# Optimization experiments

Hardware: AMD Instinct MI355X
Metric: run time of the kernel (lower is better)

The kernel has to match this reference:

```python
import jax, jax.numpy as jnp
import numpy as np

B, LC, I, H, O, T = 512, 512, 64, 100, 64, 256


def setup_inputs() -> dict:
    key = jax.random.key(0)
    ks = jax.random.split(key, 10)
    context = jax.random.normal(ks[0], (B, LC, I), dtype=jnp.float32)
    context_lengths = jnp.clip(jax.random.randint(ks[1], (B,), 0, LC), 1, LC)
    s_e = 1.0 / np.sqrt(I)   # embed init scale (pytorch Linear default)
    s_h = 1.0 / np.sqrt(H)
    u = lambda k, shp, s: jax.random.uniform(k, shp, jnp.float32, -s, s)
    return {
        "context": context,
        "context_lengths": context_lengths,
        "t_steps": T,
        "W_embed": u(ks[2], (H, I), s_e), "b_embed": u(ks[3], (H,), s_e),
        "W_ih": u(ks[4], (3 * H, H), s_h), "b_ih": u(ks[5], (3 * H,), s_h),
        "W_hh": u(ks[6], (3 * H, H), s_h), "b_hh": u(ks[7], (3 * H,), s_h),
        "W_proj": u(ks[8], (O, H), s_h), "b_proj": u(ks[9], (O,), s_h),
    }


def _gru_cell(h, x_pre, W_hh, b_hh):
    # x_pre: precomputed x @ W_ih.T + b_ih, shape [B, 3H]
    gh = h @ W_hh.T + b_hh
    ri, zi, ni = jnp.split(x_pre, 3, axis=-1)
    rh, zh, nh = jnp.split(gh, 3, axis=-1)
    r = jax.nn.sigmoid(ri + rh)
    z = jax.nn.sigmoid(zi + zh)
    n = jnp.tanh(ni + r * nh)
    return (1.0 - z) * n + z * h


def reference(context, context_lengths, t_steps, W_embed, b_embed,
              W_ih, W_hh, b_ih, b_hh, W_proj, b_proj):
    Bc = context.shape[0]
    # ---- encode ----
    x = context @ W_embed.T + b_embed                      # [B, Lc, H]
    x_pre = x @ W_ih.T + b_ih                              # [B, Lc, 3H] (input gates precomputed)

    def enc_step(h, xp):
        h = _gru_cell(h, xp, W_hh, b_hh)
        return h, h

    h_init = jnp.zeros((Bc, W_hh.shape[1]), context.dtype)
    _, hs = jax.lax.scan(enc_step, h_init, jnp.swapaxes(x_pre, 0, 1))  # hs: [Lc, B, H]
    h0 = hs[context_lengths - 1, jnp.arange(Bc)]           # last valid hidden per example

    z0 = h0 @ W_proj.T + b_proj                            # [B, O]

    def dec_step(carry, _):
        h, z = carry
        xp = (z @ W_embed.T + b_embed) @ W_ih.T + b_ih
        h = _gru_cell(h, xp, W_hh, b_hh)
        z = h @ W_proj.T + b_proj
        return (h, z), z

    _, zs = jax.lax.scan(dec_step, (h0, z0), None, length=t_steps)  # [T, B, O]
    out = jnp.concatenate([z0[None], zs], axis=0)          # [T+1, B, O]
    return jnp.swapaxes(out, 0, 1)                         # [B, T+1, O]
```

## Files before the change

kernel.cpp:

```cpp
#include <hip/hip_runtime.h>


#define B_  512
#define LC_ 512
#define I_  64
#define H_  100
#define O_  64
#define T_  256
#define H3  300

#define WS_WC   0
#define WS_BC   19200
#define WS_WD   19500
#define WS_BD   49500
#define WS_PERM 49800

typedef float v2f __attribute__((ext_vector_type(2)));

__global__ __launch_bounds__(64) void prep1(const float* __restrict__ Wih,
                                            const float* __restrict__ bih,
                                            const float* __restrict__ Wemb,
                                            const float* __restrict__ bemb,
                                            float* __restrict__ ws) {
    int j = blockIdx.x;
    int i = threadIdx.x;
    float acc = 0.f;
    for (int k = 0; k < H_; ++k) acc += Wih[j * H_ + k] * Wemb[k * I_ + i];
    ws[WS_WC + j * I_ + i] = acc;
    if (i == 0) {
        float b = bih[j];
        for (int k = 0; k < H_; ++k) b += Wih[j * H_ + k] * bemb[k];
        ws[WS_BC + j] = b;
    }
}

__global__ __launch_bounds__(128) void prep2(const float* __restrict__ Wproj,
                                             const float* __restrict__ bproj,
                                             float* __restrict__ ws) {
    int j = blockIdx.x;
    int u = threadIdx.x;
    const float* Wc = ws + WS_WC;
    if (u < H_) {
        float acc = 0.f;
        for (int o = 0; o < O_; ++o) acc += Wc[j * I_ + o] * Wproj[o * H_ + u];
        ws[WS_WD + j * H_ + u] = acc;
    }
    if (u == 0) {
        float b = ws[WS_BC + j];
        for (int o = 0; o < O_; ++o) b += Wc[j * I_ + o] * bproj[o];
        ws[WS_BD + j] = b;
    }
}

__global__ __launch_bounds__(512) void sortk(const int* __restrict__ lens,
                                             int* __restrict__ perm) {
    __shared__ int sl[B_];
    int tid = threadIdx.x;
    sl[tid] = lens[tid];
    __syncthreads();
    int li = sl[tid];
    int rank = 0;
    for (int j = 0; j < B_; ++j) {
        int lj = sl[j];
        rank += (lj > li) || (lj == li && j < tid);
    }
    perm[rank] = tid;
}

__device__ __forceinline__ float sigm_(float x) { return 1.f / (1.f + __expf(-x)); }
__device__ __forceinline__ float tanh_(float x) {
    float t = __expf(-2.f * fabsf(x));
    float r = (1.f - t) / (1.f + t);
    return (x >= 0.f) ? r : -r;
}

template <int CTRL>
__device__ __forceinline__ float dppmov_(float x) {
    return __int_as_float(
        __builtin_amdgcn_mov_dpp(__float_as_int(x), CTRL, 0xF, 0xF, true));
}
__device__ __forceinline__ float red4_(float a) {
    a += dppmov_<0xB1>(a);
    a += dppmov_<0x4E>(a);
    return a;
}

__device__ __forceinline__ float dotH_(const v2f* __restrict__ w2, float w1,
                                       const v2f* __restrict__ hv2, float h24) {
    v2f a = {0.f, 0.f};
    #pragma unroll
    for (int j = 0; j < 12; ++j) a = w2[j] * hv2[j] + a;
    return red4_(fmaf(w1, h24, a.x + a.y));
}
__device__ __forceinline__ float dotC_(const v2f* __restrict__ w2,
                                       const v2f* __restrict__ cv2) {
    v2f a = {0.f, 0.f};
    #pragma unroll
    for (int j = 0; j < 8; ++j) a = w2[j] * cv2[j] + a;
    return red4_(a.x + a.y);
}

__global__ __attribute__((amdgpu_flat_work_group_size(512, 512)))
__attribute__((amdgpu_waves_per_eu(2, 2)))
void rnn8(const float* __restrict__ ctx, const int* __restrict__ lens,
          const float* __restrict__ Whh, const float* __restrict__ bhh,
          const float* __restrict__ Wproj, const float* __restrict__ bproj,
          const float* __restrict__ ws, float* __restrict__ out) {

    const int tid = threadIdx.x;
    const int l   = tid & 3;
    const int g   = tid >> 2;
    const bool wl = (l == 0);

    const int* perm = (const int*)(ws + WS_PERM);
    const int e0 = perm[blockIdx.x];
    const int e1 = perm[511 - blockIdx.x];
    const int len0 = lens[e0], len1 = lens[e1];

    __shared__ __align__(16) float sh[2][112];
    __shared__ __align__(16) float sctx[2][64];
    __shared__ float sdot[2][672];
    __shared__ float sbh[H3], sbx[H3];

    const bool p2hh = (g < 44);
    const bool p4a  = (g < 88);
    const bool p5a  = (g < 24);

    v2f   w2[6][12];
    float w1[6];
    {
        const float* r0 = Whh + g * H_ + 25 * l;
        const float* r1 = Whh + (128 + g) * H_ + 25 * l;
        #pragma unroll
        for (int j = 0; j < 12; ++j) {
            w2[0][j] = v2f{r0[2 * j], r0[2 * j + 1]};
            w2[1][j] = v2f{r1[2 * j], r1[2 * j + 1]};
        }
        w1[0] = r0[24]; w1[1] = r1[24];
        if (p2hh) {
            const float* r2 = Whh + (256 + g) * H_ + 25 * l;
            #pragma unroll
            for (int j = 0; j < 12; ++j) w2[2][j] = v2f{r2[2 * j], r2[2 * j + 1]};
            w1[2] = r2[24];
        } else {
            const float* r2 = ws + WS_WC + (g - 44) * I_ + 16 * l;
            #pragma unroll
            for (int j = 0; j < 8; ++j) w2[2][j] = v2f{r2[2 * j], r2[2 * j + 1]};
        }
        const float* r3 = ws + WS_WC + (84 + g) * I_ + 16 * l;
        #pragma unroll
        for (int j = 0; j < 8; ++j) w2[3][j] = v2f{r3[2 * j], r3[2 * j + 1]};
        if (p4a) {
            const float* r4 = ws + WS_WC + (212 + g) * I_ + 16 * l;
            #pragma unroll
            for (int j = 0; j < 8; ++j) w2[4][j] = v2f{r4[2 * j], r4[2 * j + 1]};
        }
    }

    const int ge = (tid >= 100);
    const int gi = tid - (ge ? 100 : 0);
    const int hs = 28 * (gi / 25) + (gi % 25);
    const int lenG = ge ? len1 : len0;
    float hreg = 0.f;

    const int oe = (tid >> 6) & 1;
    const int oo = tid & 63;
    float* oute = out + (size_t)(oe ? e1 : e0) * (T_ + 1) * O_;
    float bpr = 0.f;
    if (tid >= 256 && tid < 384) bpr = bproj[oo];

    const int pe = (tid >> 4) & 1;
    const int pi = tid & 15;
    const float4* pctx = (const float4*)(ctx + (size_t)(pe ? e1 : e0) * LC_ * I_);
    const int lenP = pe ? len1 : len0;

    if (tid < 224) ((float*)sh)[tid] = 0.f;
    if (tid < H3) { sbh[tid] = bhh[tid]; sbx[tid] = (ws + WS_BC)[tid]; }
    if (tid >= 384 && tid < 416) *(float4*)&sctx[pe][4 * pi] = pctx[pi];
    __syncthreads();

    for (int t = 0; t < len0; ++t) {
        float4 pf;
        const bool hp = (tid >= 384 && tid < 416) && (t + 1 < lenP);
        if (hp) pf = pctx[(t + 1) * 16 + pi];

        #pragma unroll
        for (int e = 0; e < 2; ++e) {
            if (e == 0 || t < len1) {
                v2f hv2[12], cv2[8];
                float h24;
                #pragma unroll
                for (int q = 0; q < 6; ++q) {
                    float4 f = *(const float4*)&sh[e][28 * l + 4 * q];
                    hv2[2 * q]     = v2f{f.x, f.y};
                    hv2[2 * q + 1] = v2f{f.z, f.w};
                }
                h24 = sh[e][28 * l + 24];
                #pragma unroll
                for (int q = 0; q < 4; ++q) {
                    float4 f = *(const float4*)&sctx[e][16 * l + 4 * q];
                    cv2[2 * q]     = v2f{f.x, f.y};
                    cv2[2 * q + 1] = v2f{f.z, f.w};
                }

                float a0 = dotH_(w2[0], w1[0], hv2, h24);
                float a1 = dotH_(w2[1], w1[1], hv2, h24);
                float a2 = p2hh ? dotH_(w2[2], w1[2], hv2, h24) : dotC_(w2[2], cv2);
                float a3 = dotC_(w2[3], cv2);
                if (wl) {
                    sdot[e][g] = a0;
                    sdot[e][128 + g] = a1;
                    sdot[e][256 + g] = a2;
                    sdot[e][384 + g] = a3;
                }
                if (p4a) {
                    float a4 = dotC_(w2[4], cv2);
                    if (wl) sdot[e][512 + g] = a4;
                }
            }
        }
        __syncthreads();
        if (tid < 200 && t < lenG) {
            const float* sd = sdot[ge];
            float gr = sd[gi]       + sbh[gi];
            float gz = sd[gi + 100] + sbh[gi + 100];
            float gn = sd[gi + 200] + sbh[gi + 200];
            float xr = sd[gi + 300] + sbx[gi];
            float xz = sd[gi + 400] + sbx[gi + 100];
            float xn = sd[gi + 500] + sbx[gi + 200];
            float r = sigm_(xr + gr);
            float z = sigm_(xz + gz);
            float n = tanh_(xn + r * gn);
            hreg = (1.f - z) * n + z * hreg;
            sh[ge][hs] = hreg;
        }
        if (hp) *(float4*)&sctx[pe][4 * pi] = pf;
        __syncthreads();
    }

    {
        if (!p2hh) {
            const float* r2 = ws + WS_WD + (g - 44) * H_ + 25 * l;
            #pragma unroll
            for (int j = 0; j < 12; ++j) w2[2][j] = v2f{r2[2 * j], r2[2 * j + 1]};
            w1[2] = r2[24];
        }
        const float* r3 = ws + WS_WD + (84 + g) * H_ + 25 * l;
        #pragma unroll
        for (int j = 0; j < 12; ++j) w2[3][j] = v2f{r3[2 * j], r3[2 * j + 1]};
        w1[3] = r3[24];
        const float* r4 = p4a ? (ws + WS_WD + (212 + g) * H_ + 25 * l)
                              : (Wproj + (g - 88) * H_ + 25 * l);
        #pragma unroll
        for (int j = 0; j < 12; ++j) w2[4][j] = v2f{r4[2 * j], r4[2 * j + 1]};
        w1[4] = r4[24];
        if (p5a) {
            const float* r5 = Wproj + (40 + g) * H_ + 25 * l;
            #pragma unroll
            for (int j = 0; j < 12; ++j) w2[5][j] = v2f{r5[2 * j], r5[2 * j + 1]};
            w1[5] = r5[24];
        }
    }
    if (tid < H3) sbx[tid] = (ws + WS_BD)[tid];

    for (int t = 0; t <= T_; ++t) {
        #pragma unroll
        for (int e = 0; e < 2; ++e) {
            v2f hv2[12];
            float h24;
            #pragma unroll
            for (int q = 0; q < 6; ++q) {
                float4 f = *(const float4*)&sh[e][28 * l + 4 * q];
                hv2[2 * q]     = v2f{f.x, f.y};
                hv2[2 * q + 1] = v2f{f.z, f.w};
            }
            h24 = sh[e][28 * l + 24];

            float a0 = dotH_(w2[0], w1[0], hv2, h24);
            float a1 = dotH_(w2[1], w1[1], hv2, h24);
            float a2 = dotH_(w2[2], w1[2], hv2, h24);
            float a3 = dotH_(w2[3], w1[3], hv2, h24);
            float a4 = dotH_(w2[4], w1[4], hv2, h24);
            if (wl) {
                sdot[e][g] = a0;
                sdot[e][128 + g] = a1;
                sdot[e][256 + g] = a2;
                sdot[e][384 + g] = a3;
                sdot[e][512 + g] = a4;
            }
            if (p5a) {
                float a5 = dotH_(w2[5], w1[5], hv2, h24);
                if (wl) sdot[e][640 + g] = a5;
            }
        }
        __syncthreads();
        if (tid >= 256 && tid < 384) {
            oute[t * O_ + oo] = sdot[oe][600 + oo] + bpr;
        }
        if (t == T_) break;
        if (tid < 200) {
            const float* sd = sdot[ge];
            float gr = sd[gi]       + sbh[gi];
            float gz = sd[gi + 100] + sbh[gi + 100];
            float gn = sd[gi + 200] + sbh[gi + 200];
            float xr = sd[gi + 300] + sbx[gi];
            float xz = sd[gi + 400] + sbx[gi + 100];
            float xn = sd[gi + 500] + sbx[gi + 200];
            float r = sigm_(xr + gr);
            float z = sigm_(xz + gz);
            float n = tanh_(xn + r * gn);
            hreg = (1.f - z) * n + z * hreg;
            sh[ge][hs] = hreg;
        }
        __syncthreads();
    }
}

extern "C" void kernel_launch(void* const* d_in, const int* in_sizes, int n_in,
                              void* d_out, int out_size, void* d_ws, size_t ws_size,
                              hipStream_t stream) {
    (void)in_sizes; (void)n_in; (void)out_size; (void)ws_size;
    const float* ctx  = (const float*)d_in[0];
    const int*   lens = (const int*)d_in[1];
    const float* Wemb = (const float*)d_in[3];
    const float* bemb = (const float*)d_in[4];
    const float* Wih  = (const float*)d_in[5];
    const float* bih  = (const float*)d_in[6];
    const float* Whh  = (const float*)d_in[7];
    const float* bhh  = (const float*)d_in[8];
    const float* Wpr  = (const float*)d_in[9];
    const float* bpr  = (const float*)d_in[10];
    float* ws  = (float*)d_ws;
    float* out = (float*)d_out;

    prep1<<<H3, 64, 0, stream>>>(Wih, bih, Wemb, bemb, ws);
    prep2<<<H3, 128, 0, stream>>>(Wpr, bpr, ws);
    sortk<<<1, 512, 0, stream>>>(lens, (int*)(ws + WS_PERM));
    rnn8<<<256, 512, 0, stream>>>(ctx, lens, Whh, bhh, Wpr, bpr, ws, out);
}
```

Before: 729.2 us.

## Interleave two sequences' dot and gate phases to overlap gate math with dots

Restructures both the encoder and decoder loops so that the gate update for one sequence runs in the same barrier interval as the matrix-vector dots for the other sequence, in a staggered ping-pong. The context prefetch buffer is double-buffered per sequence to fit the new schedule. The intent is to hide the serial gate/activation phase, which previously sat between barriers with most threads idle, behind the dot-product work. It adds bookkeeping for the offset between the two sequences and a tail step, and the barrier count per step stays the same.

After: 742.4 us. Within noise of the previous version (+1.8%).

```diff
diff --git a/kernel.cpp b/kernel.cpp
--- a/kernel.cpp
+++ b/kernel.cpp
@@ -102,7 +102,7 @@
 
 __global__ __attribute__((amdgpu_flat_work_group_size(512, 512)))
 __attribute__((amdgpu_waves_per_eu(2, 2)))
-void rnn8(const float* __restrict__ ctx, const int* __restrict__ lens,
+void rnn9(const float* __restrict__ ctx, const int* __restrict__ lens,
           const float* __restrict__ Whh, const float* __restrict__ bhh,
           const float* __restrict__ Wproj, const float* __restrict__ bproj,
           const float* __restrict__ ws, float* __restrict__ out) {
@@ -118,7 +118,7 @@
     const int len0 = lens[e0], len1 = lens[e1];
 
     __shared__ __align__(16) float sh[2][112];
-    __shared__ __align__(16) float sctx[2][64];
+    __shared__ __align__(16) float sctx[2][2][64];
     __shared__ float sdot[2][672];
     __shared__ float sbh[H3], sbx[H3];
 
@@ -160,81 +160,121 @@
     const int ge = (tid >= 100);
     const int gi = tid - (ge ? 100 : 0);
     const int hs = 28 * (gi / 25) + (gi % 25);
-    const int lenG = ge ? len1 : len0;
     float hreg = 0.f;
 
-    const int oe = (tid >> 6) & 1;
+    const bool iso = (tid >= 256 && tid < 320);
     const int oo = tid & 63;
-    float* oute = out + (size_t)(oe ? e1 : e0) * (T_ + 1) * O_;
+    float* oute0 = out + (size_t)e0 * (T_ + 1) * O_;
+    float* oute1 = out + (size_t)e1 * (T_ + 1) * O_;
     float bpr = 0.f;
-    if (tid >= 256 && tid < 384) bpr = bproj[oo];
-
-    const int pe = (tid >> 4) & 1;
+    if (iso) bpr = bproj[oo];
+
+    const bool isp = (tid >= 384 && tid < 400);
     const int pi = tid & 15;
-    const float4* pctx = (const float4*)(ctx + (size_t)(pe ? e1 : e0) * LC_ * I_);
-    const int lenP = pe ? len1 : len0;
+    const float4* pctx0 = (const float4*)(ctx + (size_t)e0 * LC_ * I_);
+    const float4* pctx1 = (const float4*)(ctx + (size_t)e1 * LC_ * I_);
 
     if (tid < 224) ((float*)sh)[tid] = 0.f;
     if (tid < H3) { sbh[tid] = bhh[tid]; sbx[tid] = (ws + WS_BC)[tid]; }
-    if (tid >= 384 && tid < 416) *(float4*)&sctx[pe][4 * pi] = pctx[pi];
+    if (isp) {
+        *(float4*)&sctx[0][0][4 * pi] = pctx0[pi];
+        *(float4*)&sctx[1][0][4 * pi] = pctx1[pi];
+    }
     __syncthreads();
 
+    auto gate_ = [&](int e) {
+        const float* sd = sdot[e];
+        float gr = sd[gi]       + sbh[gi];
+        float gz = sd[gi + 100] + sbh[gi + 100];
+        float gn = sd[gi + 200] + sbh[gi + 200];
+        float xr = sd[gi + 300] + sbx[gi];
+        float xz = sd[gi + 400] + sbx[gi + 100];
+        float xn = sd[gi + 500] + sbx[gi + 200];
+        float r = sigm_(xr + gr);
+        float z = sigm_(xz + gz);
+        float n = tanh_(xn + r * gn);
+        hreg = (1.f - z) * n + z * hreg;
+        sh[e][hs] = hreg;
+    };
+    auto dotsEnc = [&](int e, int buf) {
+        v2f hv2[12], cv2[8];
+        float h24;
+        #pragma unroll
+        for (int q = 0; q < 6; ++q) {
+            float4 f = *(const float4*)&sh[e][28 * l + 4 * q];
+            hv2[2 * q]     = v2f{f.x, f.y};
+            hv2[2 * q + 1] = v2f{f.z, f.w};
+        }
+        h24 = sh[e][28 * l + 24];
+        #pragma unroll
+        for (int q = 0; q < 4; ++q) {
+            float4 f = *(const float4*)&sctx[e][buf][16 * l + 4 * q];
+            cv2[2 * q]     = v2f{f.x, f.y};
+            cv2[2 * q + 1] = v2f{f.z, f.w};
+        }
+        float a0 = dotH_(w2[0], w1[0], hv2, h24);
+        float a1 = dotH_(w2[1], w1[1], hv2, h24);
+        float a2 = p2hh ? dotH_(w2[2], w1[2], hv2, h24) : dotC_(w2[2], cv2);
+        float a3 = dotC_(w2[3], cv2);
+        if (wl) {
+            sdot[e][g] = a0;
+            sdot[e][128 + g] = a1;
+            sdot[e][256 + g] = a2;
+            sdot[e][384 + g] = a3;
+        }
+        if (p4a) {
+            float a4 = dotC_(w2[4], cv2);
+            if (wl) sdot[e][512 + g] = a4;
+        }
+    };
+    auto dotsDec = [&](int e) {
+        v2f hv2[12];
+        float h24;
+        #pragma unroll
+        for (int q = 0; q < 6; ++q) {
+            float4 f = *(const float4*)&sh[e][28 * l + 4 * q];
+            hv2[2 * q]     = v2f{f.x, f.y};
+            hv2[2 * q + 1] = v2f{f.z, f.w};
+        }
+        h24 = sh[e][28 * l + 24];
+        float a0 = dotH_(w2[0], w1[0], hv2, h24);
+        float a1 = dotH_(w2[1], w1[1], hv2, h24);
+        float a2 = dotH_(w2[2], w1[2], hv2, h24);
+        float a3 = dotH_(w2[3], w1[3], hv2, h24);
+        float a4 = dotH_(w2[4], w1[4], hv2, h24);
+        if (wl) {
+            sdot[e][g] = a0;
+            sdot[e][128 + g] = a1;
+            sdot[e][256 + g] = a2;
+            sdot[e][384 + g] = a3;
+            sdot[e][512 + g] = a4;
+        }
+        if (p5a) {
+            float a5 = dotH_(w2[5], w1[5], hv2, h24);
+            if (wl) sdot[e][640 + g] = a5;
+        }
+    };
+
+    float4 pf;
+
     for (int t = 0; t < len0; ++t) {
-        float4 pf;
-        const bool hp = (tid >= 384 && tid < 416) && (t + 1 < lenP);
-        if (hp) pf = pctx[(t + 1) * 16 + pi];
-
-        #pragma unroll
-        for (int e = 0; e < 2; ++e) {
-            if (e == 0 || t < len1) {
-                v2f hv2[12], cv2[8];
-                float h24;
-                #pragma unroll
-                for (int q = 0; q < 6; ++q) {
-                    float4 f = *(const float4*)&sh[e][28 * l + 4 * q];
-                    hv2[2 * q]     = v2f{f.x, f.y};
-                    hv2[2 * q + 1] = v2f{f.z, f.w};
-                }
-                h24 = sh[e][28 * l + 24];
-                #pragma unroll
-                for (int q = 0; q < 4; ++q) {
-                    float4 f = *(const float4*)&sctx[e][16 * l + 4 * q];
-                    cv2[2 * q]     = v2f{f.x, f.y};
-                    cv2[2 * q + 1] = v2f{f.z, f.w};
-                }
-
-                float a0 = dotH_(w2[0], w1[0], hv2, h24);
-                float a1 = dotH_(w2[1], w1[1], hv2, h24);
-                float a2 = p2hh ? dotH_(w2[2], w1[2], hv2, h24) : dotC_(w2[2], cv2);
-                float a3 = dotC_(w2[3], cv2);
-                if (wl) {
-                    sdot[e][g] = a0;
-                    sdot[e][128 + g] = a1;
-                    sdot[e][256 + g] = a2;
-                    sdot[e][384 + g] = a3;
-                }
-                if (p4a) {
-                    float a4 = dotC_(w2[4], cv2);
-                    if (wl) sdot[e][512 + g] = a4;
-                }
-            }
-        }
-        __syncthreads();
-        if (tid < 200 && t < lenG) {
-            const float* sd = sdot[ge];
-            float gr = sd[gi]       + sbh[gi];
-            float gz = sd[gi + 100] + sbh[gi + 100];
-            float gn = sd[gi + 200] + sbh[gi + 200];
-            float xr = sd[gi + 300] + sbx[gi];
-            float xz = sd[gi + 400] + sbx[gi + 100];
-            float xn = sd[gi + 500] + sbx[gi + 200];
-            float r = sigm_(xr + gr);
-            float z = sigm_(xz + gz);
-            float n = tanh_(xn + r * gn);
-            hreg = (1.f - z) * n + z * hreg;
-            sh[ge][hs] = hreg;
-        }
-        if (hp) *(float4*)&sctx[pe][4 * pi] = pf;
+        if (isp) {
+            if (t >= 1 && t < len1) *(float4*)&sctx[1][t & 1][4 * pi] = pf;
+            if (t + 1 < len0) pf = pctx0[(t + 1) * 16 + pi];
+        }
+        if (ge && tid < 200 && t >= 1 && t - 1 < len1) gate_(1);
+        dotsEnc(0, t & 1);
+        __syncthreads();
+        if (isp) {
+            if (t + 1 < len0) *(float4*)&sctx[0][(t + 1) & 1][4 * pi] = pf;
+            if (t + 1 < len1) pf = pctx1[(t + 1) * 16 + pi];
+        }
+        if (tid < 100) gate_(0);
+        if (t < len1) dotsEnc(1, t & 1);
+        __syncthreads();
+    }
+    if (len1 == len0) {
+        if (ge && tid < 200) gate_(1);
         __syncthreads();
     }
 
@@ -264,56 +304,18 @@
     if (tid < H3) sbx[tid] = (ws + WS_BD)[tid];
 
     for (int t = 0; t <= T_; ++t) {
-        #pragma unroll
-        for (int e = 0; e < 2; ++e) {
-            v2f hv2[12];
-            float h24;
-            #pragma unroll
-            for (int q = 0; q < 6; ++q) {
-                float4 f = *(const float4*)&sh[e][28 * l + 4 * q];
-                hv2[2 * q]     = v2f{f.x, f.y};
-                hv2[2 * q + 1] = v2f{f.z, f.w};
-            }
-            h24 = sh[e][28 * l + 24];
-
-            float a0 = dotH_(w2[0], w1[0], hv2, h24);
-            float a1 = dotH_(w2[1], w1[1], hv2, h24);
-            float a2 = dotH_(w2[2], w1[2], hv2, h24);
-            float a3 = dotH_(w2[3], w1[3], hv2, h24);
-            float a4 = dotH_(w2[4], w1[4], hv2, h24);
-            if (wl) {
-                sdot[e][g] = a0;
-                sdot[e][128 + g] = a1;
-                sdot[e][256 + g] = a2;
-                sdot[e][384 + g] = a3;
-                sdot[e][512 + g] = a4;
-            }
-            if (p5a) {
-                float a5 = dotH_(w2[5], w1[5], hv2, h24);
-                if (wl) sdot[e][640 + g] = a5;
-            }
-        }
-        __syncthreads();
-        if (tid >= 256 && tid < 384) {
-            oute[t * O_ + oo] = sdot[oe][600 + oo] + bpr;
-        }
-        if (t == T_) break;
-        if (tid < 200) {
-            const float* sd = sdot[ge];
-            float gr = sd[gi]       + sbh[gi];
-            float gz = sd[gi + 100] + sbh[gi + 100];
-            float gn = sd[gi + 200] + sbh[gi + 200];
-            float xr = sd[gi + 300] + sbx[gi];
-            float xz = sd[gi + 400] + sbx[gi + 100];
-            float xn = sd[gi + 500] + sbx[gi + 200];
-            float r = sigm_(xr + gr);
-            float z = sigm_(xz + gz);
-            float n = tanh_(xn + r * gn);
-            hreg = (1.f - z) * n + z * hreg;
-            sh[ge][hs] = hreg;
-        }
-        __syncthreads();
-    }
+        if (t >= 1) {
+            if (ge && tid < 200) gate_(1);
+            if (iso) oute1[(t - 1) * O_ + oo] = sdot[1][600 + oo] + bpr;
+        }
+        dotsDec(0);
+        __syncthreads();
+        if (tid < 100 && t < T_) gate_(0);
+        if (iso) oute0[t * O_ + oo] = sdot[0][600 + oo] + bpr;
+        dotsDec(1);
+        __syncthreads();
+    }
+    if (iso) oute1[T_ * O_ + oo] = sdot[1][600 + oo] + bpr;
 }
 
 extern "C" void kernel_launch(void* const* d_in, const int* in_sizes, int n_in,
@@ -336,5 +338,5 @@
     prep1<<<H3, 64, 0, stream>>>(Wih, bih, Wemb, bemb, ws);
     prep2<<<H3, 128, 0, stream>>>(Wpr, bpr, ws);
     sortk<<<1, 512, 0, stream>>>(lens, (int*)(ws + WS_PERM));
-    rnn8<<<256, 512, 0, stream>>>(ctx, lens, Whh, bhh, Wpr, bpr, ws, out);
-}
+    rnn9<<<256, 512, 0, stream>>>(ctx, lens, Whh, bhh, Wpr, bpr, ws, out);
+}
```

## Fuse gate math into per-row dot threads with double-buffered hidden state

Applied to the files above, without the earlier changes.

Restructures the recurrent kernel so each 4-lane group owns one hidden unit and holds all six gate weight rows plus biases in registers. The group computes the gate nonlinearities and the new hidden value directly, with no shared-memory dot-product scratch. Hidden state and context are double-buffered, which cuts each timestep from two barriers to one. The projection output moves to a separate set of 64 threads that compute it alongside the next step. The cost is higher register pressure from the extra weight rows and redundant gate math across the four lanes.

Measured after the change: 1.382 ms. 89.5% more time.

```diff
diff --git a/kernel.cpp b/kernel.cpp
--- a/kernel.cpp
+++ b/kernel.cpp
@@ -102,10 +102,10 @@
 
 __global__ __attribute__((amdgpu_flat_work_group_size(512, 512)))
 __attribute__((amdgpu_waves_per_eu(2, 2)))
-void rnn8(const float* __restrict__ ctx, const int* __restrict__ lens,
-          const float* __restrict__ Whh, const float* __restrict__ bhh,
-          const float* __restrict__ Wproj, const float* __restrict__ bproj,
-          const float* __restrict__ ws, float* __restrict__ out) {
+void rnn10(const float* __restrict__ ctx, const int* __restrict__ lens,
+           const float* __restrict__ Whh, const float* __restrict__ bhh,
+           const float* __restrict__ Wproj, const float* __restrict__ bproj,
+           const float* __restrict__ ws, float* __restrict__ out) {
 
     const int tid = threadIdx.x;
     const int l   = tid & 3;
@@ -117,200 +117,199 @@
     const int e1 = perm[511 - blockIdx.x];
     const int len0 = lens[e0], len1 = lens[e1];
 
-    __shared__ __align__(16) float sh[2][112];
-    __shared__ __align__(16) float sctx[2][64];
-    __shared__ float sdot[2][672];
-    __shared__ float sbh[H3], sbx[H3];
-
-    const bool p2hh = (g < 44);
-    const bool p4a  = (g < 88);
-    const bool p5a  = (g < 24);
-
-    v2f   w2[6][12];
-    float w1[6];
-    {
-        const float* r0 = Whh + g * H_ + 25 * l;
-        const float* r1 = Whh + (128 + g) * H_ + 25 * l;
+    __shared__ __align__(16) float sh[2][2][112];
+    __shared__ __align__(16) float sctx[2][2][64];
+
+    const bool isG  = (g < 112);
+    const bool real = (g < 100);
+    const int  hslot = real ? (28 * (g / 25) + (g % 25)) : 0;
+
+    v2f   wh[3][12]; float wh1[3]; float bh[3];
+    v2f   wx[3][12]; float wx1[3]; float bx[3];
+    float hreg0 = 0.f, hreg1 = 0.f;
+    v2f   wp[4][12]; float wp1[4]; float bp[4];
+
+    if (isG) {
         #pragma unroll
-        for (int j = 0; j < 12; ++j) {
-            w2[0][j] = v2f{r0[2 * j], r0[2 * j + 1]};
-            w2[1][j] = v2f{r1[2 * j], r1[2 * j + 1]};
-        }
-        w1[0] = r0[24]; w1[1] = r1[24];
-        if (p2hh) {
-            const float* r2 = Whh + (256 + g) * H_ + 25 * l;
+        for (int r = 0; r < 3; ++r) {
+            if (real) {
+                const float* p = Whh + (g + 100 * r) * H_ + 25 * l;
+                #pragma unroll
+                for (int j = 0; j < 12; ++j) wh[r][j] = v2f{p[2 * j], p[2 * j + 1]};
+                wh1[r] = p[24];
+                bh[r]  = bhh[g + 100 * r];
+                const float* pc = ws + WS_WC + (g + 100 * r) * I_ + 16 * l;
+                #pragma unroll
+                for (int j = 0; j < 8; ++j) wx[r][j] = v2f{pc[2 * j], pc[2 * j + 1]};
+                bx[r] = ws[WS_BC + g + 100 * r];
+            } else {
+                #pragma unroll
+                for (int j = 0; j < 12; ++j) { wh[r][j] = v2f{0.f, 0.f}; wx[r][j] = v2f{0.f, 0.f}; }
+                wh1[r] = 0.f; wx1[r] = 0.f; bh[r] = 0.f; bx[r] = 0.f;
+            }
+        }
+    } else {
+        const int k = g - 112;
+        #pragma unroll
+        for (int r = 0; r < 4; ++r) {
+            const float* p = Wproj + (k + 16 * r) * H_ + 25 * l;
             #pragma unroll
-            for (int j = 0; j < 12; ++j) w2[2][j] = v2f{r2[2 * j], r2[2 * j + 1]};
-            w1[2] = r2[24];
-        } else {
-            const float* r2 = ws + WS_WC + (g - 44) * I_ + 16 * l;
-            #pragma unroll
-            for (int j = 0; j < 8; ++j) w2[2][j] = v2f{r2[2 * j], r2[2 * j + 1]};
-        }
-        const float* r3 = ws + WS_WC + (84 + g) * I_ + 16 * l;
+            for (int j = 0; j < 12; ++j) wp[r][j] = v2f{p[2 * j], p[2 * j + 1]};
+            wp1[r] = p[24];
+            bp[r]  = bproj[k + 16 * r];
+        }
+    }
+
+    const int pl = tid - 448;
+    const int pe = (pl >> 4) & 1;
+    const int pi = pl & 15;
+    const float4* pc0 = (const float4*)(ctx + (size_t)e0 * LC_ * I_);
+    const float4* pc1 = (const float4*)(ctx + (size_t)e1 * LC_ * I_);
+    const float4* pcm = pe ? pc1 : pc0;
+    const int lenp = pe ? len1 : len0;
+    float4 pf = {0.f, 0.f, 0.f, 0.f};
+
+    float* oute0 = out + (size_t)e0 * (T_ + 1) * O_;
+    float* oute1 = out + (size_t)e1 * (T_ + 1) * O_;
+
+    if (tid < 448) ((float*)sh)[tid] = 0.f;
+    if (!isG && pl < 32) {
+        *(float4*)&sctx[pe][0][4 * pi] = pcm[pi];
+        if (1 < lenp) pf = pcm[16 + pi];
+    }
+    __syncthreads();
+
+    auto loadH = [&](int e, int b, v2f* hv2, float& h24) {
         #pragma unroll
-        for (int j = 0; j < 8; ++j) w2[3][j] = v2f{r3[2 * j], r3[2 * j + 1]};
-        if (p4a) {
-            const float* r4 = ws + WS_WC + (212 + g) * I_ + 16 * l;
-            #pragma unroll
-            for (int j = 0; j < 8; ++j) w2[4][j] = v2f{r4[2 * j], r4[2 * j + 1]};
-        }
-    }
-
-    const int ge = (tid >= 100);
-    const int gi = tid - (ge ? 100 : 0);
-    const int hs = 28 * (gi / 25) + (gi % 25);
-    const int lenG = ge ? len1 : len0;
-    float hreg = 0.f;
-
-    const int oe = (tid >> 6) & 1;
-    const int oo = tid & 63;
-    float* oute = out + (size_t)(oe ? e1 : e0) * (T_ + 1) * O_;
-    float bpr = 0.f;
-    if (tid >= 256 && tid < 384) bpr = bproj[oo];
-
-    const int pe = (tid >> 4) & 1;
-    const int pi = tid & 15;
-    const float4* pctx = (const float4*)(ctx + (size_t)(pe ? e1 : e0) * LC_ * I_);
-    const int lenP = pe ? len1 : len0;
-
-    if (tid < 224) ((float*)sh)[tid] = 0.f;
-    if (tid < H3) { sbh[tid] = bhh[tid]; sbx[tid] = (ws + WS_BC)[tid]; }
-    if (tid >= 384 && tid < 416) *(float4*)&sctx[pe][4 * pi] = pctx[pi];
-    __syncthreads();
+        for (int q = 0; q < 6; ++q) {
+            float4 f = *(const float4*)&sh[e][b][28 * l + 4 * q];
+            hv2[2 * q]     = v2f{f.x, f.y};
+            hv2[2 * q + 1] = v2f{f.z, f.w};
+        }
+        h24 = sh[e][b][28 * l + 24];
+    };
 
     for (int t = 0; t < len0; ++t) {
-        float4 pf;
-        const bool hp = (tid >= 384 && tid < 416) && (t + 1 < lenP);
-        if (hp) pf = pctx[(t + 1) * 16 + pi];
-
-        #pragma unroll
-        for (int e = 0; e < 2; ++e) {
-            if (e == 0 || t < len1) {
-                v2f hv2[12], cv2[8];
-                float h24;
-                #pragma unroll
-                for (int q = 0; q < 6; ++q) {
-                    float4 f = *(const float4*)&sh[e][28 * l + 4 * q];
-                    hv2[2 * q]     = v2f{f.x, f.y};
-                    hv2[2 * q + 1] = v2f{f.z, f.w};
-                }
-                h24 = sh[e][28 * l + 24];
+        const int rb = t & 1, wb = rb ^ 1;
+        if (isG) {
+            {
+                v2f hv2[12], cv2[8]; float h24;
+                loadH(0, rb, hv2, h24);
                 #pragma unroll
                 for (int q = 0; q < 4; ++q) {
-                    float4 f = *(const float4*)&sctx[e][16 * l + 4 * q];
+                    float4 f = *(const float4*)&sctx[0][rb][16 * l + 4 * q];
                     cv2[2 * q]     = v2f{f.x, f.y};
                     cv2[2 * q + 1] = v2f{f.z, f.w};
                 }
-
-                float a0 = dotH_(w2[0], w1[0], hv2, h24);
-                float a1 = dotH_(w2[1], w1[1], hv2, h24);
-                float a2 = p2hh ? dotH_(w2[2], w1[2], hv2, h24) : dotC_(w2[2], cv2);
-                float a3 = dotC_(w2[3], cv2);
-                if (wl) {
-                    sdot[e][g] = a0;
-                    sdot[e][128 + g] = a1;
-                    sdot[e][256 + g] = a2;
-                    sdot[e][384 + g] = a3;
+                float gr = dotH_(wh[0], wh1[0], hv2, h24) + bh[0];
+                float gz = dotH_(wh[1], wh1[1], hv2, h24) + bh[1];
+                float gn = dotH_(wh[2], wh1[2], hv2, h24) + bh[2];
+                float xr = dotC_(wx[0], cv2) + bx[0];
+                float xz = dotC_(wx[1], cv2) + bx[1];
+                float xn = dotC_(wx[2], cv2) + bx[2];
+                float r = sigm_(xr + gr);
+                float z = sigm_(xz + gz);
+                float n = tanh_(xn + r * gn);
+                hreg0 = (1.f - z) * n + z * hreg0;
+                if (wl && real) sh[0][wb][hslot] = hreg0;
+            }
+            if (t < len1) {
+                v2f hv2[12], cv2[8]; float h24;
+                loadH(1, rb, hv2, h24);
+                #pragma unroll
+                for (int q = 0; q < 4; ++q) {
+                    float4 f = *(const float4*)&sctx[1][rb][16 * l + 4 * q];
+                    cv2[2 * q]     = v2f{f.x, f.y};
+                    cv2[2 * q + 1] = v2f{f.z, f.w};
                 }
-                if (p4a) {
-                    float a4 = dotC_(w2[4], cv2);
-                    if (wl) sdot[e][512 + g] = a4;
+                float gr = dotH_(wh[0], wh1[0], hv2, h24) + bh[0];
+                float gz = dotH_(wh[1], wh1[1], hv2, h24) + bh[1];
+                float gn = dotH_(wh[2], wh1[2], hv2, h24) + bh[2];
+                float xr = dotC_(wx[0], cv2) + bx[0];
+                float xz = dotC_(wx[1], cv2) + bx[1];
+                float xn = dotC_(wx[2], cv2) + bx[2];
+                float r = sigm_(xr + gr);
+                float z = sigm_(xz + gz);
+                float n = tanh_(xn + r * gn);
+                hreg1 = (1.f - z) * n + z * hreg1;
+                if (wl && real) sh[1][wb][hslot] = hreg1;
+            }
+        } else if (pl < 32) {
+            if (t + 1 < lenp) *(float4*)&sctx[pe][wb][4 * pi] = pf;
+            if (t + 2 < lenp) pf = pcm[(t + 2) * 16 + pi];
+        }
+        __syncthreads();
+    }
+
+    if (isG && real) {
+        #pragma unroll
+        for (int r = 0; r < 3; ++r) {
+            const float* p = ws + WS_WD + (g + 100 * r) * H_ + 25 * l;
+            #pragma unroll
+            for (int j = 0; j < 12; ++j) wx[r][j] = v2f{p[2 * j], p[2 * j + 1]};
+            wx1[r] = p[24];
+            bx[r]  = ws[WS_BD + g + 100 * r];
+        }
+    }
+
+    const int p0 = len0 & 1, p1 = len1 & 1;
+    for (int t = 0; t <= T_; ++t) {
+        const int rb0 = (p0 + t) & 1, rb1 = (p1 + t) & 1;
+        if (isG) {
+            if (t < T_) {
+                {
+                    v2f hv2[12]; float h24;
+                    loadH(0, rb0, hv2, h24);
+                    float gr = dotH_(wh[0], wh1[0], hv2, h24) + bh[0];
+                    float gz = dotH_(wh[1], wh1[1], hv2, h24) + bh[1];
+                    float gn = dotH_(wh[2], wh1[2], hv2, h24) + bh[2];
+                    float xr = dotH_(wx[0], wx1[0], hv2, h24) + bx[0];
+                    float xz = dotH_(wx[1], wx1[1], hv2, h24) + bx[1];
+                    float xn = dotH_(wx[2], wx1[2], hv2, h24) + bx[2];
+                    float r = sigm_(xr + gr);
+                    float z = sigm_(xz + gz);
+                    float n = tanh_(xn + r * gn);
+                    hreg0 = (1.f - z) * n + z * hreg0;
+                    if (wl && real) sh[0][rb0 ^ 1][hslot] = hreg0;
                 }
-            }
-        }
-        __syncthreads();
-        if (tid < 200 && t < lenG) {
-            const float* sd = sdot[ge];
-            float gr = sd[gi]       + sbh[gi];
-            float gz = sd[gi + 100] + sbh[gi + 100];
-            float gn = sd[gi + 200] + sbh[gi + 200];
-            float xr = sd[gi + 300] + sbx[gi];
-            float xz = sd[gi + 400] + sbx[gi + 100];
-            float xn = sd[gi + 500] + sbx[gi + 200];
-            float r = sigm_(xr + gr);
-            float z = sigm_(xz + gz);
-            float n = tanh_(xn + r * gn);
-            hreg = (1.f - z) * n + z * hreg;
-            sh[ge][hs] = hreg;
-        }
-        if (hp) *(float4*)&sctx[pe][4 * pi] = pf;
-        __syncthreads();
-    }
-
-    {
-        if (!p2hh) {
-            const float* r2 = ws + WS_WD + (g - 44) * H_ + 25 * l;
-            #pragma unroll
-            for (int j = 0; j < 12; ++j) w2[2][j] = v2f{r2[2 * j], r2[2 * j + 1]};
-            w1[2] = r2[24];
-        }
-        const float* r3 = ws + WS_WD + (84 + g) * H_ + 25 * l;
-        #pragma unroll
-        for (int j = 0; j < 12; ++j) w2[3][j] = v2f{r3[2 * j], r3[2 * j + 1]};
-        w1[3] = r3[24];
-        const float* r4 = p4a ? (ws + WS_WD + (212 + g) * H_ + 25 * l)
-                              : (Wproj + (g - 88) * H_ + 25 * l);
-        #pragma unroll
-        for (int j = 0; j < 12; ++j) w2[4][j] = v2f{r4[2 * j], r4[2 * j + 1]};
-        w1[4] = r4[24];
-        if (p5a) {
-            const float* r5 = Wproj + (40 + g) * H_ + 25 * l;
-            #pragma unroll
-            for (int j = 0; j < 12; ++j) w2[5][j] = v2f{r5[2 * j], r5[2 * j + 1]};
-            w1[5] = r5[24];
-        }
-    }
-    if (tid < H3) sbx[tid] = (ws + WS_BD)[tid];
-
-    for (int t = 0; t <= T_; ++t) {
-        #pragma unroll
-        for (int e = 0; e < 2; ++e) {
-            v2f hv2[12];
-            float h24;
-            #pragma unroll
-            for (int q = 0; q < 6; ++q) {
-                float4 f = *(const float4*)&sh[e][28 * l + 4 * q];
-                hv2[2 * q]     = v2f{f.x, f.y};
-                hv2[2 * q + 1] = v2f{f.z, f.w};
-            }
-            h24 = sh[e][28 * l + 24];
-
-            float a0 = dotH_(w2[0], w1[0], hv2, h24);
-            float a1 = dotH_(w2[1], w1[1], hv2, h24);
-            float a2 = dotH_(w2[2], w1[2], hv2, h24);
-            float a3 = dotH_(w2[3], w1[3], hv2, h24);
-            float a4 = dotH_(w2[4], w1[4], hv2, h24);
-            if (wl) {
-                sdot[e][g] = a0;
-                sdot[e][128 + g] = a1;
-                sdot[e][256 + g] = a2;
-                sdot[e][384 + g] = a3;
-                sdot[e][512 + g] = a4;
-            }
-            if (p5a) {
-                float a5 = dotH_(w2[5], w1[5], hv2, h24);
-                if (wl) sdot[e][640 + g] = a5;
-            }
-        }
-        __syncthreads();
-        if (tid >= 256 && tid < 384) {
-            oute[t * O_ + oo] = sdot[oe][600 + oo] + bpr;
-        }
-        if (t == T_) break;
-        if (tid < 200) {
-            const float* sd = sdot[ge];
-            float gr = sd[gi]       + sbh[gi];
-            float gz = sd[gi + 100] + sbh[gi + 100];
-            float gn = sd[gi + 200] + sbh[gi + 200];
-            float xr = sd[gi + 300] + sbx[gi];
-            float xz = sd[gi + 400] + sbx[gi + 100];
-            float xn = sd[gi + 500] + sbx[gi + 200];
-            float r = sigm_(xr + gr);
-            float z = sigm_(xz + gz);
-            float n = tanh_(xn + r * gn);
-            hreg = (1.f - z) * n + z * hreg;
-            sh[ge][hs] = hreg;
+                {
+                    v2f hv2[12]; float h24;
+                    loadH(1, rb1, hv2, h24);
+                    float gr = dotH_(wh[0], wh1[0], hv2, h24) + bh[0];
+                    float gz = dotH_(wh[1], wh1[1], hv2, h24) + bh[1];
+                    float gn = dotH_(wh[2], wh1[2], hv2, h24) + bh[2];
+                    float xr = dotH_(wx[0], wx1[0], hv2, h24) + bx[0];
+                    float xz = dotH_(wx[1], wx1[1], hv2, h24) + bx[1];
+                    float xn = dotH_(wx[2], wx1[2], hv2, h24) + bx[2];
+                    float r = sigm_(xr + gr);
+                    float z = sigm_(xz + gz);
+                    float n = tanh_(xn + r * gn);
+                    hreg1 = (1.f - z) * n + z * hreg1;
+                    if (wl && real) sh[1][rb1 ^ 1][hslot] = hreg1;
+                }
+            }
+        } else {
+            const int k = g - 112;
+            {
+                v2f hv2[12]; float h24;
+                loadH(0, rb0, hv2, h24);
+                float s0 = dotH_(wp[0], wp1[0], hv2, h24) + bp[0];
+                float s1 = dotH_(wp[1], wp1[1], hv2, h24) + bp[1];
+                float s2 = dotH_(wp[2], wp1[2], hv2, h24) + bp[2];
+                float s3 = dotH_(wp[3], wp1[3], hv2, h24) + bp[3];
+                float v = (l == 0) ? s0 : (l == 1) ? s1 : (l == 2) ? s2 : s3;
+                oute0[t * O_ + k + 16 * l] = v;
+            }
+            {
+                v2f hv2[12]; float h24;
+                loadH(1, rb1, hv2, h24);
+                float s0 = dotH_(wp[0], wp1[0], hv2, h24) + bp[0];
+                float s1 = dotH_(wp[1], wp1[1], hv2, h24) + bp[1];
+                float s2 = dotH_(wp[2], wp1[2], hv2, h24) + bp[2];
+                float s3 = dotH_(wp[3], wp1[3], hv2, h24) + bp[3];
+                float v = (l == 0) ? s0 : (l == 1) ? s1 : (l == 2) ? s2 : s3;
+                oute1[t * O_ + k + 16 * l] = v;
+            }
         }
         __syncthreads();
     }
@@ -336,5 +335,5 @@
     prep1<<<H3, 64, 0, stream>>>(Wih, bih, Wemb, bemb, ws);
     prep2<<<H3, 128, 0, stream>>>(Wpr, bpr, ws);
     sortk<<<1, 512, 0, stream>>>(lens, (int*)(ws + WS_PERM));
-    rnn8<<<256, 512, 0, stream>>>(ctx, lens, Whh, bhh, Wpr, bpr, ws, out);
-}
+    rnn10<<<256, 512, 0, stream>>>(ctx, lens, Whh, bhh, Wpr, bpr, ws, out);
+}
```

## Repartition GRU matvec across 8-lane groups with 11 rows per thread

Applied to the files above, without the earlier changes.

The recurrent kernel's work split changes. Each output row used to be computed by 4 lanes over 25 columns, with up to 6 rows per thread. Now 8 lanes each take 13 columns, and each thread holds 10–11 consecutive rows: recurrent, context-input, decoder-input and projection rows in one slot array. Partial sums are reduced only within 4 lanes, so the two half-sums are written as vectorised float4 stores into two shared buffers and added in the gate stage. The aim is a shorter per-step critical path and fewer scalar shared-memory stores, at the cost of more index arithmetic, padded loads and an extra add per gate.

After: 1.174 ms. 1.61x slower.

```diff
diff --git a/kernel.cpp b/kernel.cpp
--- a/kernel.cpp
+++ b/kernel.cpp
@@ -85,86 +85,92 @@
     return a;
 }
 
-__device__ __forceinline__ float dotH_(const v2f* __restrict__ w2, float w1,
-                                       const v2f* __restrict__ hv2, float h24) {
+__device__ __forceinline__ float dotH8_(const v2f* __restrict__ w, float wt,
+                                        const v2f* __restrict__ hv, float h12) {
     v2f a = {0.f, 0.f};
     #pragma unroll
-    for (int j = 0; j < 12; ++j) a = w2[j] * hv2[j] + a;
-    return red4_(fmaf(w1, h24, a.x + a.y));
-}
-__device__ __forceinline__ float dotC_(const v2f* __restrict__ w2,
-                                       const v2f* __restrict__ cv2) {
+    for (int j = 0; j < 6; ++j) a = w[j] * hv[j] + a;
+    return red4_(fmaf(wt, h12, a.x + a.y));
+}
+__device__ __forceinline__ float dotC8_(const v2f* __restrict__ w,
+                                        const v2f* __restrict__ cv) {
     v2f a = {0.f, 0.f};
     #pragma unroll
-    for (int j = 0; j < 8; ++j) a = w2[j] * cv2[j] + a;
+    for (int j = 0; j < 4; ++j) a = w[j] * cv[j] + a;
     return red4_(a.x + a.y);
+}
+
+__device__ __forceinline__ int slotOf_(int r) {
+    return (r < 264) ? 12 * (r / 11) + (r % 11)
+                     : 12 * (24 + (r - 264) / 10) + ((r - 264) % 10);
+}
+
+__device__ __forceinline__ void loadH13_(const float* __restrict__ p, int c0,
+                                         v2f* __restrict__ w, float& wt) {
+    #pragma unroll
+    for (int j = 0; j < 6; ++j) {
+        float a = (c0 + 2 * j     < H_) ? p[2 * j]     : 0.f;
+        float b = (c0 + 2 * j + 1 < H_) ? p[2 * j + 1] : 0.f;
+        w[j] = v2f{a, b};
+    }
+    wt = (c0 + 12 < H_) ? p[12] : 0.f;
 }
 
 __global__ __attribute__((amdgpu_flat_work_group_size(512, 512)))
 __attribute__((amdgpu_waves_per_eu(2, 2)))
-void rnn8(const float* __restrict__ ctx, const int* __restrict__ lens,
-          const float* __restrict__ Whh, const float* __restrict__ bhh,
-          const float* __restrict__ Wproj, const float* __restrict__ bproj,
-          const float* __restrict__ ws, float* __restrict__ out) {
+void rnn15(const float* __restrict__ ctx, const int* __restrict__ lens,
+           const float* __restrict__ Whh, const float* __restrict__ bhh,
+           const float* __restrict__ Wproj, const float* __restrict__ bproj,
+           const float* __restrict__ ws, float* __restrict__ out) {
 
     const int tid = threadIdx.x;
-    const int l   = tid & 3;
-    const int g   = tid >> 2;
-    const bool wl = (l == 0);
+    const int l8  = tid & 7;
+    const int g8  = tid >> 3;
 
     const int* perm = (const int*)(ws + WS_PERM);
     const int e0 = perm[blockIdx.x];
     const int e1 = perm[511 - blockIdx.x];
     const int len0 = lens[e0], len1 = lens[e1];
 
-    __shared__ __align__(16) float sh[2][112];
+    __shared__ __align__(16) float sh[2][140];
     __shared__ __align__(16) float sctx[2][64];
-    __shared__ float sdot[2][672];
+    __shared__ __align__(16) float sd2[2][2][768];
     __shared__ float sbh[H3], sbx[H3];
 
-    const bool p2hh = (g < 44);
-    const bool p4a  = (g < 88);
-    const bool p5a  = (g < 24);
-
-    v2f   w2[6][12];
-    float w1[6];
-    {
-        const float* r0 = Whh + g * H_ + 25 * l;
-        const float* r1 = Whh + (128 + g) * H_ + 25 * l;
-        #pragma unroll
-        for (int j = 0; j < 12; ++j) {
-            w2[0][j] = v2f{r0[2 * j], r0[2 * j + 1]};
-            w2[1][j] = v2f{r1[2 * j], r1[2 * j + 1]};
-        }
-        w1[0] = r0[24]; w1[1] = r1[24];
-        if (p2hh) {
-            const float* r2 = Whh + (256 + g) * H_ + 25 * l;
-            #pragma unroll
-            for (int j = 0; j < 12; ++j) w2[2][j] = v2f{r2[2 * j], r2[2 * j + 1]};
-            w1[2] = r2[24];
-        } else {
-            const float* r2 = ws + WS_WC + (g - 44) * I_ + 16 * l;
-            #pragma unroll
-            for (int j = 0; j < 8; ++j) w2[2][j] = v2f{r2[2 * j], r2[2 * j + 1]};
-        }
-        const float* r3 = ws + WS_WC + (84 + g) * I_ + 16 * l;
-        #pragma unroll
-        for (int j = 0; j < 8; ++j) w2[3][j] = v2f{r3[2 * j], r3[2 * j + 1]};
-        if (p4a) {
-            const float* r4 = ws + WS_WC + (212 + g) * I_ + 16 * l;
-            #pragma unroll
-            for (int j = 0; j < 8; ++j) w2[4][j] = v2f{r4[2 * j], r4[2 * j + 1]};
+    const int cnt   = (g8 < 24) ? 11 : 10;
+    const int start = (g8 < 24) ? 11 * g8 : 264 + 10 * (g8 - 24);
+    int nH = 300 - start; nH = nH < 0 ? 0 : (nH > 11 ? 11 : nH);
+    int nC = 600 - start; nC = nC < 0 ? 0 : (nC > 11 ? 11 : nC);
+
+    v2f   wS[11][6];
+    float w1v[11];
+    const int c0 = 13 * l8;
+    #pragma unroll
+    for (int i = 0; i < 11; ++i) {
+        if (i < cnt) {
+            int row = start + i;
+            if (row < 300) {
+                loadH13_(Whh + row * H_ + c0, c0, wS[i], w1v[i]);
+            } else if (row < 600) {
+                const float* p = ws + WS_WC + (row - 300) * I_ + 8 * l8;
+                #pragma unroll
+                for (int j = 0; j < 4; ++j) wS[i][j] = v2f{p[2 * j], p[2 * j + 1]};
+            }
         }
     }
 
     const int ge = (tid >= 100);
     const int gi = tid - (ge ? 100 : 0);
-    const int hs = 28 * (gi / 25) + (gi % 25);
+    const int gch = gi / 13;
+    const int hG = 16 * gch + 4 * (gch >> 1) + (gi % 13);
+    const int sG0 = slotOf_(gi),       sG1 = slotOf_(gi + 100), sG2 = slotOf_(gi + 200);
+    const int sG3 = slotOf_(gi + 300), sG4 = slotOf_(gi + 400), sG5 = slotOf_(gi + 500);
     const int lenG = ge ? len1 : len0;
     float hreg = 0.f;
 
     const int oe = (tid >> 6) & 1;
     const int oo = tid & 63;
+    const int spr = slotOf_(600 + oo);
     float* oute = out + (size_t)(oe ? e1 : e0) * (T_ + 1) * O_;
     float bpr = 0.f;
     if (tid >= 256 && tid < 384) bpr = bproj[oo];
@@ -174,10 +180,29 @@
     const float4* pctx = (const float4*)(ctx + (size_t)(pe ? e1 : e0) * LC_ * I_);
     const int lenP = pe ? len1 : len0;
 
-    if (tid < 224) ((float*)sh)[tid] = 0.f;
+    if (tid < 280) ((float*)sh)[tid] = 0.f;
     if (tid < H3) { sbh[tid] = bhh[tid]; sbx[tid] = (ws + WS_BC)[tid]; }
     if (tid >= 384 && tid < 416) *(float4*)&sctx[pe][4 * pi] = pctx[pi];
     __syncthreads();
+
+    const int hO = 16 * l8 + 4 * (l8 >> 1);
+    auto loadHv = [&](int e, v2f* hv, float& h12) {
+        const float* hb = sh[e];
+        float4 f0 = *(const float4*)(hb + hO);
+        float4 f1 = *(const float4*)(hb + hO + 4);
+        float4 f2 = *(const float4*)(hb + hO + 8);
+        hv[0] = v2f{f0.x, f0.y}; hv[1] = v2f{f0.z, f0.w};
+        hv[2] = v2f{f1.x, f1.y}; hv[3] = v2f{f1.z, f1.w};
+        hv[4] = v2f{f2.x, f2.y}; hv[5] = v2f{f2.z, f2.w};
+        h12 = hb[hO + 12];
+    };
+    auto loadCv = [&](int e, v2f* cv) {
+        const float* cb = sctx[e] + 8 * l8;
+        float4 f0 = *(const float4*)(cb);
+        float4 f1 = *(const float4*)(cb + 4);
+        cv[0] = v2f{f0.x, f0.y}; cv[1] = v2f{f0.z, f0.w};
+        cv[2] = v2f{f1.x, f1.y}; cv[3] = v2f{f1.z, f1.w};
+    };
 
     for (int t = 0; t < len0; ++t) {
         float4 pf;
@@ -187,78 +212,56 @@
         #pragma unroll
         for (int e = 0; e < 2; ++e) {
             if (e == 0 || t < len1) {
-                v2f hv2[12], cv2[8];
-                float h24;
-                #pragma unroll
-                for (int q = 0; q < 6; ++q) {
-                    float4 f = *(const float4*)&sh[e][28 * l + 4 * q];
-                    hv2[2 * q]     = v2f{f.x, f.y};
-                    hv2[2 * q + 1] = v2f{f.z, f.w};
-                }
-                h24 = sh[e][28 * l + 24];
-                #pragma unroll
-                for (int q = 0; q < 4; ++q) {
-                    float4 f = *(const float4*)&sctx[e][16 * l + 4 * q];
-                    cv2[2 * q]     = v2f{f.x, f.y};
-                    cv2[2 * q + 1] = v2f{f.z, f.w};
-                }
-
-                float a0 = dotH_(w2[0], w1[0], hv2, h24);
-                float a1 = dotH_(w2[1], w1[1], hv2, h24);
-                float a2 = p2hh ? dotH_(w2[2], w1[2], hv2, h24) : dotC_(w2[2], cv2);
-                float a3 = dotC_(w2[3], cv2);
-                if (wl) {
-                    sdot[e][g] = a0;
-                    sdot[e][128 + g] = a1;
-                    sdot[e][256 + g] = a2;
-                    sdot[e][384 + g] = a3;
-                }
-                if (p4a) {
-                    float a4 = dotC_(w2[4], cv2);
-                    if (wl) sdot[e][512 + g] = a4;
+                v2f hv[6]; float h12; v2f cv[4];
+                loadHv(e, hv, h12);
+                loadCv(e, cv);
+                #define ENC_DOT(i) ((i) < nH ? dotH8_(wS[i], w1v[i], hv, h12) \
+                                   : ((i) < nC ? dotC8_(wS[i], cv) : 0.f))
+                float rr0 = ENC_DOT(0), rr1 = ENC_DOT(1), rr2 = ENC_DOT(2);
+                float rr3 = ENC_DOT(3), rr4 = ENC_DOT(4), rr5 = ENC_DOT(5);
+                float rr6 = ENC_DOT(6), rr7 = ENC_DOT(7), rr8 = ENC_DOT(8);
+                float rr9 = ENC_DOT(9);
+                #undef ENC_DOT
+                float rr10 = 0.f;
+                if (tid < 192) rr10 = dotH8_(wS[10], w1v[10], hv, h12);
+                if ((l8 & 3) == 0) {
+                    float* bp = &sd2[l8 >> 2][e][12 * g8];
+                    *(float4*)(bp)     = make_float4(rr0, rr1, rr2, rr3);
+                    *(float4*)(bp + 4) = make_float4(rr4, rr5, rr6, rr7);
+                    *(float2*)(bp + 8) = make_float2(rr8, rr9);
+                    if (tid < 192) bp[10] = rr10;
                 }
             }
         }
         __syncthreads();
         if (tid < 200 && t < lenG) {
-            const float* sd = sdot[ge];
-            float gr = sd[gi]       + sbh[gi];
-            float gz = sd[gi + 100] + sbh[gi + 100];
-            float gn = sd[gi + 200] + sbh[gi + 200];
-            float xr = sd[gi + 300] + sbx[gi];
-            float xz = sd[gi + 400] + sbx[gi + 100];
-            float xn = sd[gi + 500] + sbx[gi + 200];
+            const float* A = sd2[0][ge];
+            const float* Bb = sd2[1][ge];
+            float gr = A[sG0] + Bb[sG0] + sbh[gi];
+            float gz = A[sG1] + Bb[sG1] + sbh[gi + 100];
+            float gn = A[sG2] + Bb[sG2] + sbh[gi + 200];
+            float xr = A[sG3] + Bb[sG3] + sbx[gi];
+            float xz = A[sG4] + Bb[sG4] + sbx[gi + 100];
+            float xn = A[sG5] + Bb[sG5] + sbx[gi + 200];
             float r = sigm_(xr + gr);
             float z = sigm_(xz + gz);
             float n = tanh_(xn + r * gn);
             hreg = (1.f - z) * n + z * hreg;
-            sh[ge][hs] = hreg;
+            sh[ge][hG] = hreg;
         }
         if (hp) *(float4*)&sctx[pe][4 * pi] = pf;
         __syncthreads();
     }
 
-    {
-        if (!p2hh) {
-            const float* r2 = ws + WS_WD + (g - 44) * H_ + 25 * l;
-            #pragma unroll
-            for (int j = 0; j < 12; ++j) w2[2][j] = v2f{r2[2 * j], r2[2 * j + 1]};
-            w1[2] = r2[24];
-        }
-        const float* r3 = ws + WS_WD + (84 + g) * H_ + 25 * l;
-        #pragma unroll
-        for (int j = 0; j < 12; ++j) w2[3][j] = v2f{r3[2 * j], r3[2 * j + 1]};
-        w1[3] = r3[24];
-        const float* r4 = p4a ? (ws + WS_WD + (212 + g) * H_ + 25 * l)
-                              : (Wproj + (g - 88) * H_ + 25 * l);
-        #pragma unroll
-        for (int j = 0; j < 12; ++j) w2[4][j] = v2f{r4[2 * j], r4[2 * j + 1]};
-        w1[4] = r4[24];
-        if (p5a) {
-            const float* r5 = Wproj + (40 + g) * H_ + 25 * l;
-            #pragma unroll
-            for (int j = 0; j < 12; ++j) w2[5][j] = v2f{r5[2 * j], r5[2 * j + 1]};
-            w1[5] = r5[24];
+    #pragma unroll
+    for (int i = 0; i < 11; ++i) {
+        if (i < cnt) {
+            int row = start + i;
+            if (row >= 300) {
+                const float* p = (row < 600) ? (ws + WS_WD + (row - 300) * H_)
+                                             : (Wproj + (row - 600) * H_);
+                loadH13_(p + c0, c0, wS[i], w1v[i]);
+            }
         }
     }
     if (tid < H3) sbx[tid] = (ws + WS_BD)[tid];
@@ -266,51 +269,47 @@
     for (int t = 0; t <= T_; ++t) {
         #pragma unroll
         for (int e = 0; e < 2; ++e) {
-            v2f hv2[12];
-            float h24;
-            #pragma unroll
-            for (int q = 0; q < 6; ++q) {
-                float4 f = *(const float4*)&sh[e][28 * l + 4 * q];
-                hv2[2 * q]     = v2f{f.x, f.y};
-                hv2[2 * q + 1] = v2f{f.z, f.w};
-            }
-            h24 = sh[e][28 * l + 24];
-
-            float a0 = dotH_(w2[0], w1[0], hv2, h24);
-            float a1 = dotH_(w2[1], w1[1], hv2, h24);
-            float a2 = dotH_(w2[2], w1[2], hv2, h24);
-            float a3 = dotH_(w2[3], w1[3], hv2, h24);
-            float a4 = dotH_(w2[4], w1[4], hv2, h24);
-            if (wl) {
-                sdot[e][g] = a0;
-                sdot[e][128 + g] = a1;
-                sdot[e][256 + g] = a2;
-                sdot[e][384 + g] = a3;
-                sdot[e][512 + g] = a4;
-            }
-            if (p5a) {
-                float a5 = dotH_(w2[5], w1[5], hv2, h24);
-                if (wl) sdot[e][640 + g] = a5;
+            v2f hv[6]; float h12;
+            loadHv(e, hv, h12);
+            float rr0 = dotH8_(wS[0], w1v[0], hv, h12);
+            float rr1 = dotH8_(wS[1], w1v[1], hv, h12);
+            float rr2 = dotH8_(wS[2], w1v[2], hv, h12);
+            float rr3 = dotH8_(wS[3], w1v[3], hv, h12);
+            float rr4 = dotH8_(wS[4], w1v[4], hv, h12);
+            float rr5 = dotH8_(wS[5], w1v[5], hv, h12);
+            float rr6 = dotH8_(wS[6], w1v[6], hv, h12);
+            float rr7 = dotH8_(wS[7], w1v[7], hv, h12);
+            float rr8 = dotH8_(wS[8], w1v[8], hv, h12);
+            float rr9 = dotH8_(wS[9], w1v[9], hv, h12);
+            float rr10 = 0.f;
+            if (tid < 192) rr10 = dotH8_(wS[10], w1v[10], hv, h12);
+            if ((l8 & 3) == 0) {
+                float* bp = &sd2[l8 >> 2][e][12 * g8];
+                *(float4*)(bp)     = make_float4(rr0, rr1, rr2, rr3);
+                *(float4*)(bp + 4) = make_float4(rr4, rr5, rr6, rr7);
+                *(float2*)(bp + 8) = make_float2(rr8, rr9);
+                if (tid < 192) bp[10] = rr10;
             }
         }
         __syncthreads();
         if (tid >= 256 && tid < 384) {
-            oute[t * O_ + oo] = sdot[oe][600 + oo] + bpr;
+            oute[t * O_ + oo] = sd2[0][oe][spr] + sd2[1][oe][spr] + bpr;
         }
         if (t == T_) break;
         if (tid < 200) {
-            const float* sd = sdot[ge];
-            float gr = sd[gi]       + sbh[gi];
-            float gz = sd[gi + 100] + sbh[gi + 100];
-            float gn = sd[gi + 200] + sbh[gi + 200];
-            float xr = sd[gi + 300] + sbx[gi];
-            float xz = sd[gi + 400] + sbx[gi + 100];
-            float xn = sd[gi + 500] + sbx[gi + 200];
+            const float* A = sd2[0][ge];
+            const float* Bb = sd2[1][ge];
+            float gr = A[sG0] + Bb[sG0] + sbh[gi];
+            float gz = A[sG1] + Bb[sG1] + sbh[gi + 100];
+            float gn = A[sG2] + Bb[sG2] + sbh[gi + 200];
+            float xr = A[sG3] + Bb[sG3] + sbx[gi];
+            float xz = A[sG4] + Bb[sG4] + sbx[gi + 100];
+            float xn = A[sG5] + Bb[sG5] + sbx[gi + 200];
             float r = sigm_(xr + gr);
             float z = sigm_(xz + gz);
             float n = tanh_(xn + r * gn);
             hreg = (1.f - z) * n + z * hreg;
-            sh[ge][hs] = hreg;
+            sh[ge][hG] = hreg;
         }
         __syncthreads();
     }
@@ -336,5 +335,5 @@
     prep1<<<H3, 64, 0, stream>>>(Wih, bih, Wemb, bemb, ws);
     prep2<<<H3, 128, 0, stream>>>(Wpr, bpr, ws);
     sortk<<<1, 512, 0, stream>>>(lens, (int*)(ws + WS_PERM));
-    rnn8<<<256, 512, 0, stream>>>(ctx, lens, Whh, bhh, Wpr, bpr, ws, out);
-}
+    rnn15<<<256, 512, 0, stream>>>(ctx, lens, Whh, bhh, Wpr, bpr, ws, out);
+}
```
